# Kernel tuning notes

Measured on AMD Instinct MI355X. Metric: run time of the kernel, lower is better.

## Reference

```python
import jax, jax.numpy as jnp
import numpy as np

STACK = 4

def setup_inputs() -> dict:
    key = jax.random.key(0)
    k1, k2, k3 = jax.random.split(key, 3)
    b, t, c = 16, 3000, 80
    proj_dim, num_codes = 16, 8192
    x = jax.random.normal(k1, (b, t, c), dtype=jnp.float32)
    # xavier_uniform for proj: bound = sqrt(6/(fan_in+fan_out))
    fan_in, fan_out = c * STACK, proj_dim
    bound = float(np.sqrt(6.0 / (fan_in + fan_out)))
    proj = jax.random.uniform(k2, (fan_in, proj_dim), dtype=jnp.float32,
                              minval=-bound, maxval=bound)
    codebook = jax.random.normal(k3, (num_codes, proj_dim), dtype=jnp.float32)
    return {"x": x, "proj": proj, "codebook": codebook}

def _l2norm(v, axis=-1, eps=1e-12):
    # matches torch F.normalize(dim=-1)
    n = jnp.sqrt(jnp.sum(v * v, axis=axis, keepdims=True))
    return v / jnp.maximum(n, eps)

def reference(x, proj, codebook):
    b, t, c = x.shape
    if STACK > 1:
        pad = (STACK - t % STACK) % STACK
        if pad:
            x = jnp.pad(x, ((0, 0), (0, pad), (0, 0)))
            t = x.shape[1]
        x = x.reshape(b, t // STACK, c * STACK)
    x_proj = _l2norm(x @ proj)                 # (b, t', proj_dim)
    cb = _l2norm(codebook)                     # (num_codes, proj_dim)
    # ||a-c||^2 = ||a||^2 + ||c||^2 - 2 a.c = 2 - 2 a.c for unit vectors;
    # avoids materializing the (b, t', num_codes, proj_dim) diff tensor.
    scores = jnp.einsum('btd,nd->btn', x_proj, cb)  # (b, t', num_codes)
    dist = 2.0 - 2.0 * scores
    return jnp.argmin(dist, axis=-1)
```

## Files before the change

kernel.cpp:

```cpp
#include <hip/hip_runtime.h>


#define ROWS   12000
#define DIN    320
#define PD     16
#define NCODES 8192

#define NSL    8
#define SLC    (NCODES/NSL)
#define RT     6
#define RPB    48
#define NRG    (ROWS/RPB)
#define GRID   (NRG*NSL)

typedef unsigned long long u64;

__global__ __launch_bounds__(256) void prep_pt(const float* __restrict__ proj,
                                               float* __restrict__ projT) {
    int gt = blockIdx.x * 256 + threadIdx.x;
    if (gt < DIN * PD) {
        int k = gt >> 4, p = gt & 15;
        projT[p * DIN + k] = proj[k * PD + p];
    }
}

__global__ __launch_bounds__(256) void prep_cb(const float* __restrict__ cb,
                                               float* __restrict__ cbt) {
    int gt = blockIdx.x * 256 + threadIdx.x;
    int n = gt >> 4, p = gt & 15;
    float v = cb[gt];
    float ss = v * v;
    ss += __shfl_xor(ss, 1, 16);
    ss += __shfl_xor(ss, 2, 16);
    ss += __shfl_xor(ss, 4, 16);
    ss += __shfl_xor(ss, 8, 16);
    float nrm = fmaxf(sqrtf(ss), 1e-12f);
    int s = n >> 10, cl = n & 1023, q = p >> 2, j = p & 3;
    cbt[s * 16384 + q * 4096 + cl * 4 + j] = v / nrm;
}

__global__ __launch_bounds__(256) void prep_xp(const float* __restrict__ x,
                                               const float* __restrict__ projT,
                                               float* __restrict__ xp) {
    int gt = blockIdx.x * 256 + threadIdx.x;
    int r = gt >> 4, p = gt & 15;
    const float4* xr = reinterpret_cast<const float4*>(x + (size_t)r * DIN);
    const float4* pt = reinterpret_cast<const float4*>(projT + (size_t)p * DIN);
    float acc = 0.f;
#pragma unroll 8
    for (int k4 = 0; k4 < DIN / 4; ++k4) {
        float4 xv = xr[k4];
        float4 pv = pt[k4];
        acc = fmaf(xv.x, pv.x, acc);
        acc = fmaf(xv.y, pv.y, acc);
        acc = fmaf(xv.z, pv.z, acc);
        acc = fmaf(xv.w, pv.w, acc);
    }
    float ss = acc * acc;
    ss += __shfl_xor(ss, 1, 16);
    ss += __shfl_xor(ss, 2, 16);
    ss += __shfl_xor(ss, 4, 16);
    ss += __shfl_xor(ss, 8, 16);
    xp[gt] = acc / fmaxf(sqrtf(ss), 1e-12f);
}

__global__ __launch_bounds__(256)
__attribute__((amdgpu_waves_per_eu(2, 2)))
void rpq_main(const float* __restrict__ xp,
              const float* __restrict__ cbt,
              u64* __restrict__ keys) {
    __shared__ __align__(16) float4 lds4[SLC * PD / 4];

    const int tid   = threadIdx.x;
    const int cs    = tid & 31;
    const int rs    = tid >> 5;
    const int slice = blockIdx.x & (NSL - 1);
    const int rg    = blockIdx.x >> 3;
    const int row0  = rg * RPB + rs * RT;

    {
        const float4* src = reinterpret_cast<const float4*>(cbt) + (size_t)slice * (SLC * PD / 4);
#pragma unroll
        for (int it = 0; it < 16; ++it)
            lds4[it * 256 + tid] = src[it * 256 + tid];
    }

    float4 xq[RT][4];
#pragma unroll
    for (int r = 0; r < RT; ++r) {
        const float4* s4 = reinterpret_cast<const float4*>(xp + (size_t)(row0 + r) * PD);
#pragma unroll
        for (int q = 0; q < 4; ++q) xq[r][q] = s4[q];
    }

    float bd[RT];
    int   bi[RT];
#pragma unroll
    for (int r = 0; r < RT; ++r) { bd[r] = 3.0e38f; bi[r] = 0; }

    __syncthreads();

    const float4* base = lds4 + cs;
    const int code_base = slice * SLC;

#pragma unroll 4
    for (int i = 0; i < SLC / 32; ++i) {
        const float4 c0 = base[i * 32 +    0];
        const float4 c1 = base[i * 32 + 1024];
        const float4 c2 = base[i * 32 + 2048];
        const float4 c3 = base[i * 32 + 3072];
        const int gcode = code_base + i * 32 + cs;
#pragma unroll
        for (int r = 0; r < RT; ++r) {
            float s = 0.f;
            s = fmaf(xq[r][0].x, c0.x, s); s = fmaf(xq[r][0].y, c0.y, s);
            s = fmaf(xq[r][0].z, c0.z, s); s = fmaf(xq[r][0].w, c0.w, s);
            s = fmaf(xq[r][1].x, c1.x, s); s = fmaf(xq[r][1].y, c1.y, s);
            s = fmaf(xq[r][1].z, c1.z, s); s = fmaf(xq[r][1].w, c1.w, s);
            s = fmaf(xq[r][2].x, c2.x, s); s = fmaf(xq[r][2].y, c2.y, s);
            s = fmaf(xq[r][2].z, c2.z, s); s = fmaf(xq[r][2].w, c2.w, s);
            s = fmaf(xq[r][3].x, c3.x, s); s = fmaf(xq[r][3].y, c3.y, s);
            s = fmaf(xq[r][3].z, c3.z, s); s = fmaf(xq[r][3].w, c3.w, s);
            float dd = 2.0f - 2.0f * s;
            if (dd < bd[r]) { bd[r] = dd; bi[r] = gcode; }
        }
    }

#pragma unroll
    for (int r = 0; r < RT; ++r) {
        unsigned ub = __float_as_uint(bd[r]);
        ub = (ub & 0x80000000u) ? ~ub : (ub | 0x80000000u);
        u64 key = ((u64)ub << 32) | (unsigned)bi[r];
#pragma unroll
        for (int off = 16; off >= 1; off >>= 1) {
            u64 o = __shfl_xor(key, off, 32);
            key = (o < key) ? o : key;
        }
        if (cs == 0) keys[(size_t)slice * ROWS + row0 + r] = key;
    }
}

__global__ __launch_bounds__(256) void rpq_reduce(const u64* __restrict__ keys,
                                                  int* __restrict__ out) {
    int r = blockIdx.x * 256 + threadIdx.x;
    if (r >= ROWS) return;
    u64 m = keys[r];
#pragma unroll
    for (int s = 1; s < NSL; ++s) {
        u64 o = keys[(size_t)s * ROWS + r];
        m = (o < m) ? o : m;
    }
    out[r] = (int)(m & 0xFFFFFFFFu);
}

extern "C" void kernel_launch(void* const* d_in, const int* in_sizes, int n_in,
                              void* d_out, int out_size, void* d_ws, size_t ws_size,
                              hipStream_t stream) {
    const float* x    = (const float*)d_in[0];
    const float* proj = (const float*)d_in[1];
    const float* cb   = (const float*)d_in[2];
    int* out = (int*)d_out;

    float* cbt   = (float*)d_ws;
    float* xp    = (float*)((char*)d_ws + 524288);
    float* projT = (float*)((char*)d_ws + 524288 + 786432);
    u64*   keys  = (u64*)  ((char*)d_ws + 524288 + 786432 + 32768);

    prep_pt<<<(DIN * PD + 255) / 256, 256, 0, stream>>>(proj, projT);
    prep_cb<<<(NCODES * PD) / 256, 256, 0, stream>>>(cb, cbt);
    prep_xp<<<(ROWS * PD) / 256, 256, 0, stream>>>(x, projT, xp);
    rpq_main<<<GRID, 256, 0, stream>>>(xp, cbt, keys);
    rpq_reduce<<<(ROWS + 255) / 256, 256, 0, stream>>>(keys, out);
}
```

Before: 147.1 us.

## Fuse prep kernels, double codebook slices, fold reduction into main via atomic counter

Result: slower. 507.5 us (+245.1%).

```diff
diff --git a/kernel.cpp b/kernel.cpp
--- a/kernel.cpp
+++ b/kernel.cpp
@@ -6,82 +6,92 @@
 #define PD     16
 #define NCODES 8192
 
-#define NSL    8
+#define NSL    16
 #define SLC    (NCODES/NSL)
 #define RT     6
 #define RPB    48
 #define NRG    (ROWS/RPB)
 #define GRID   (NRG*NSL)
 
+#define CBBLK  512
+#define XPBLK  750
+#define PSTR   324
+
 typedef unsigned long long u64;
 
-__global__ __launch_bounds__(256) void prep_pt(const float* __restrict__ proj,
-                                               float* __restrict__ projT) {
-    int gt = blockIdx.x * 256 + threadIdx.x;
-    if (gt < DIN * PD) {
-        int k = gt >> 4, p = gt & 15;
-        projT[p * DIN + k] = proj[k * PD + p];
+__global__ __launch_bounds__(256) void prep_fused(const float* __restrict__ cb,
+                                                  const float* __restrict__ proj,
+                                                  const float* __restrict__ x,
+                                                  float* __restrict__ cbt,
+                                                  float* __restrict__ xp) {
+    __shared__ __align__(16) float ldsT[PD * PSTR];
+    const int b = blockIdx.x, tid = threadIdx.x;
+
+    if (b < CBBLK) {
+        int gt = b * 256 + tid;
+        int n = gt >> 4, p = gt & 15;
+        float v = cb[gt];
+        float ss = v * v;
+        ss += __shfl_xor(ss, 1, 16);
+        ss += __shfl_xor(ss, 2, 16);
+        ss += __shfl_xor(ss, 4, 16);
+        ss += __shfl_xor(ss, 8, 16);
+        float nrm = fmaxf(sqrtf(ss), 1e-12f);
+        int s = n >> 9, cl = n & 511, q = p >> 2, j = p & 3;
+        cbt[s * 8192 + q * 2048 + cl * 4 + j] = v / nrm;
+    } else {
+#pragma unroll
+        for (int it = 0; it < 20; ++it) {
+            int g = it * 256 + tid;
+            ldsT[(g & 15) * PSTR + (g >> 4)] = proj[g];
+        }
+        __syncthreads();
+
+        const int r = (b - CBBLK) * 16 + (tid >> 4);
+        const int p = tid & 15;
+        const float4* xr = reinterpret_cast<const float4*>(x + (size_t)r * DIN);
+        const float4* pc = reinterpret_cast<const float4*>(ldsT + p * PSTR);
+
+        float acc = 0.f;
+#pragma unroll 4
+        for (int k4 = 0; k4 < DIN / 4; ++k4) {
+            float4 xv = xr[k4];
+            float4 pv = pc[k4];
+            acc = fmaf(xv.x, pv.x, acc);
+            acc = fmaf(xv.y, pv.y, acc);
+            acc = fmaf(xv.z, pv.z, acc);
+            acc = fmaf(xv.w, pv.w, acc);
+        }
+        float ss = acc * acc;
+        ss += __shfl_xor(ss, 1, 16);
+        ss += __shfl_xor(ss, 2, 16);
+        ss += __shfl_xor(ss, 4, 16);
+        ss += __shfl_xor(ss, 8, 16);
+        xp[r * PD + p] = acc / fmaxf(sqrtf(ss), 1e-12f);
     }
 }
 
-__global__ __launch_bounds__(256) void prep_cb(const float* __restrict__ cb,
-                                               float* __restrict__ cbt) {
-    int gt = blockIdx.x * 256 + threadIdx.x;
-    int n = gt >> 4, p = gt & 15;
-    float v = cb[gt];
-    float ss = v * v;
-    ss += __shfl_xor(ss, 1, 16);
-    ss += __shfl_xor(ss, 2, 16);
-    ss += __shfl_xor(ss, 4, 16);
-    ss += __shfl_xor(ss, 8, 16);
-    float nrm = fmaxf(sqrtf(ss), 1e-12f);
-    int s = n >> 10, cl = n & 1023, q = p >> 2, j = p & 3;
-    cbt[s * 16384 + q * 4096 + cl * 4 + j] = v / nrm;
-}
-
-__global__ __launch_bounds__(256) void prep_xp(const float* __restrict__ x,
-                                               const float* __restrict__ projT,
-                                               float* __restrict__ xp) {
-    int gt = blockIdx.x * 256 + threadIdx.x;
-    int r = gt >> 4, p = gt & 15;
-    const float4* xr = reinterpret_cast<const float4*>(x + (size_t)r * DIN);
-    const float4* pt = reinterpret_cast<const float4*>(projT + (size_t)p * DIN);
-    float acc = 0.f;
-#pragma unroll 8
-    for (int k4 = 0; k4 < DIN / 4; ++k4) {
-        float4 xv = xr[k4];
-        float4 pv = pt[k4];
-        acc = fmaf(xv.x, pv.x, acc);
-        acc = fmaf(xv.y, pv.y, acc);
-        acc = fmaf(xv.z, pv.z, acc);
-        acc = fmaf(xv.w, pv.w, acc);
-    }
-    float ss = acc * acc;
-    ss += __shfl_xor(ss, 1, 16);
-    ss += __shfl_xor(ss, 2, 16);
-    ss += __shfl_xor(ss, 4, 16);
-    ss += __shfl_xor(ss, 8, 16);
-    xp[gt] = acc / fmaxf(sqrtf(ss), 1e-12f);
-}
-
 __global__ __launch_bounds__(256)
-__attribute__((amdgpu_waves_per_eu(2, 2)))
+__attribute__((amdgpu_waves_per_eu(3, 3)))
 void rpq_main(const float* __restrict__ xp,
               const float* __restrict__ cbt,
-              u64* __restrict__ keys) {
+              u64* __restrict__ keys,
+              unsigned* __restrict__ cnt,
+              int* __restrict__ out) {
     __shared__ __align__(16) float4 lds4[SLC * PD / 4];
+    __shared__ unsigned dflag;
 
     const int tid   = threadIdx.x;
     const int cs    = tid & 31;
     const int rs    = tid >> 5;
     const int slice = blockIdx.x & (NSL - 1);
-    const int rg    = blockIdx.x >> 3;
+    const int rg    = blockIdx.x >> 4;
     const int row0  = rg * RPB + rs * RT;
 
     {
         const float4* src = reinterpret_cast<const float4*>(cbt) + (size_t)slice * (SLC * PD / 4);
 #pragma unroll
-        for (int it = 0; it < 16; ++it)
+        for (int it = 0; it < 8; ++it)
             lds4[it * 256 + tid] = src[it * 256 + tid];
     }
 
@@ -106,9 +116,9 @@
 #pragma unroll 4
     for (int i = 0; i < SLC / 32; ++i) {
         const float4 c0 = base[i * 32 +    0];
-        const float4 c1 = base[i * 32 + 1024];
-        const float4 c2 = base[i * 32 + 2048];
-        const float4 c3 = base[i * 32 + 3072];
+        const float4 c1 = base[i * 32 +  512];
+        const float4 c2 = base[i * 32 + 1024];
+        const float4 c3 = base[i * 32 + 1536];
         const int gcode = code_base + i * 32 + cs;
 #pragma unroll
         for (int r = 0; r < RT; ++r) {
@@ -138,19 +148,25 @@
         }
         if (cs == 0) keys[(size_t)slice * ROWS + row0 + r] = key;
     }
-}
 
-__global__ __launch_bounds__(256) void rpq_reduce(const u64* __restrict__ keys,
-                                                  int* __restrict__ out) {
-    int r = blockIdx.x * 256 + threadIdx.x;
-    if (r >= ROWS) return;
-    u64 m = keys[r];
+    __threadfence();
+    __syncthreads();
+    if (tid == 0)
+        dflag = (atomicAdd(&cnt[rg], 1u) == NSL - 1) ? 1u : 0u;
+    __syncthreads();
+    if (dflag) {
+        __threadfence();
+        if (tid < RPB) {
+            int row = rg * RPB + tid;
+            u64 m = keys[row];
 #pragma unroll
-    for (int s = 1; s < NSL; ++s) {
-        u64 o = keys[(size_t)s * ROWS + r];
-        m = (o < m) ? o : m;
+            for (int s2 = 1; s2 < NSL; ++s2) {
+                u64 o = keys[(size_t)s2 * ROWS + row];
+                m = (o < m) ? o : m;
+            }
+            out[row] = (int)(m & 0xFFFFFFFFu);
+        }
     }
-    out[r] = (int)(m & 0xFFFFFFFFu);
 }
 
 extern "C" void kernel_launch(void* const* d_in, const int* in_sizes, int n_in,
@@ -161,14 +177,12 @@
     const float* cb   = (const float*)d_in[2];
     int* out = (int*)d_out;
 
-    float* cbt   = (float*)d_ws;
-    float* xp    = (float*)((char*)d_ws + 524288);
-    float* projT = (float*)((char*)d_ws + 524288 + 786432);
-    u64*   keys  = (u64*)  ((char*)d_ws + 524288 + 786432 + 32768);
+    float*    cbt  = (float*)d_ws;
+    float*    xp   = (float*)((char*)d_ws + 524288);
+    u64*      keys = (u64*)  ((char*)d_ws + 524288 + 786432);
+    unsigned* cnt  = (unsigned*)((char*)d_ws + 524288 + 786432 + 1536000);
 
-    prep_pt<<<(DIN * PD + 255) / 256, 256, 0, stream>>>(proj, projT);
-    prep_cb<<<(NCODES * PD) / 256, 256, 0, stream>>>(cb, cbt);
-    prep_xp<<<(ROWS * PD) / 256, 256, 0, stream>>>(x, projT, xp);
-    rpq_main<<<GRID, 256, 0, stream>>>(xp, cbt, keys);
-    rpq_reduce<<<(ROWS + 255) / 256, 256, 0, stream>>>(keys, out);
+    hipMemsetAsync(cnt, 0, NRG * sizeof(unsigned), stream);
+    prep_fused<<<CBBLK + XPBLK, 256, 0, stream>>>(cb, proj, x, cbt, xp);
+    rpq_main<<<GRID, 256, 0, stream>>>(xp, cbt, keys, cnt, out);
 }
```
